# Performance work log

Hardware: AMD Instinct MI355X
Metric: run time of the kernel (lower is better)

## Reference

```python
import jax, jax.numpy as jnp
import numpy as np

B, N, C = 2, 2048, 1024
H = 16
D = C // H  # 64 head_dim
SCALE = D ** -0.5


def setup_inputs() -> dict:
    key = jax.random.key(0)
    k1, k2, k3 = jax.random.split(key, 3)
    x = jax.random.normal(k1, (B, N, C), dtype=jnp.float32)
    w_qkv = jax.random.normal(k2, (C, 3 * C), dtype=jnp.float32) * (C ** -0.5)
    w_proj = jax.random.normal(k3, (C, C), dtype=jnp.float32) * (C ** -0.5)
    b_proj = jnp.zeros((C,), dtype=jnp.float32)
    return {"x": x, "w_qkv": w_qkv, "w_proj": w_proj, "b_proj": b_proj}


def reference(x, w_qkv, w_proj, b_proj):
    # qkv projection (no bias, qkv_bias=False)
    qkv = x @ w_qkv                                   # [B,N,3C]
    qkv = qkv.reshape(B, N, 3, H, D)
    qkv = jnp.transpose(qkv, (2, 0, 3, 1, 4))         # [3,B,H,N,D]
    q, k, v = qkv[0], qkv[1], qkv[2]
    # scaled dot-product attention (full softmax == chunked loop in original)
    scores = jnp.einsum('bhqd,bhkd->bhqk', q, k) * SCALE
    attn = jax.nn.softmax(scores, axis=-1)
    out = jnp.einsum('bhqk,bhkd->bhqd', attn, v)      # [B,H,N,D]
    out = jnp.transpose(out, (0, 2, 1, 3)).reshape(B, N, C)
    return out @ w_proj + b_proj
```

## Files before the change

### kernel.cpp

```cpp
#include <hip/hip_runtime.h>
#include <stdint.h>

typedef float f32x4 __attribute__((ext_vector_type(4)));
typedef float f32x16 __attribute__((ext_vector_type(16)));
typedef __bf16 bf16x8 __attribute__((ext_vector_type(8)));
typedef unsigned int u32x4 __attribute__((ext_vector_type(4)));
typedef unsigned short u16x4 __attribute__((ext_vector_type(4)));

#define DEV __device__ __forceinline__

#define QSCALE_LOG2E 0.18033688011112042f

DEV unsigned short f2bf(float f) {
    unsigned u = __builtin_bit_cast(unsigned, f);
    u += 0x7fffu + ((u >> 16) & 1u);
    return (unsigned short)(u >> 16);
}

DEV unsigned pack2bf(float a, float b) {
    unsigned short ua = __builtin_bit_cast(unsigned short, (__bf16)a);
    unsigned short ub = __builtin_bit_cast(unsigned short, (__bf16)b);
    return (unsigned)ua | ((unsigned)ub << 16);
}

DEV void pswap(unsigned& a, unsigned& b) {
    asm volatile("v_permlane32_swap_b32 %0, %1" : "+v"(a), "+v"(b));
}

DEV void gload16(const void* g, void* l) {
    __builtin_amdgcn_global_load_lds(
        (const __attribute__((address_space(1))) unsigned int*)(uintptr_t)g,
        (__attribute__((address_space(3))) unsigned int*)(unsigned int)(uintptr_t)l,
        16, 0, 0);
}

__global__ void k_cvt(const float* __restrict__ in, unsigned short* __restrict__ out, int n4) {
    int i = blockIdx.x * 256 + threadIdx.x;
    int st = gridDim.x * 256;
    for (; i < n4; i += st) {
        f32x4 v = *(const f32x4*)(in + (size_t)i * 4);
        u16x4 o;
        o[0] = f2bf(v[0]); o[1] = f2bf(v[1]); o[2] = f2bf(v[2]); o[3] = f2bf(v[3]);
        *(u16x4*)(out + (size_t)i * 4) = o;
    }
}

__global__ void k_transpose(const float* __restrict__ in, unsigned short* __restrict__ out, int Nc) {
    __shared__ unsigned short tl[64][68];
    int n0 = blockIdx.x * 64, k0 = blockIdx.y * 64;
#pragma unroll
    for (int i = 0; i < 16; i++) {
        int idx = i * 256 + threadIdx.x;
        int kr = idx >> 6, nc = idx & 63;
        tl[kr][nc] = f2bf(in[(size_t)(k0 + kr) * Nc + n0 + nc]);
    }
    __syncthreads();
#pragma unroll
    for (int i = 0; i < 8; i++) {
        int idx = i * 256 + threadIdx.x;
        int nr = idx >> 5, kp2 = idx & 31;
        unsigned vv = (unsigned)tl[kp2 * 2][nr] | ((unsigned)tl[kp2 * 2 + 1][nr] << 16);
        *(unsigned*)(out + (size_t)(n0 + nr) * 1024 + k0 + kp2 * 2) = vv;
    }
}

template <int MODE>
__global__ __launch_bounds__(256) void k_gemm(
    const unsigned short* __restrict__ A, const unsigned short* __restrict__ Bt, int K,
    unsigned short* __restrict__ q, unsigned short* __restrict__ kk_,
    unsigned short* __restrict__ vT, const float* __restrict__ bias,
    float* __restrict__ outf) {
    __shared__ unsigned short As[2][128 * 64];
    __shared__ unsigned short Bs[2][128 * 64];
    const int tid = threadIdx.x;
    const int w = tid >> 6, l = tid & 63, g = l >> 4, lr = l & 15;
    const int wr = w >> 1, wc = w & 1;
    const int nwg = gridDim.x * gridDim.y, cpx = nwg >> 3;
    const int lin = blockIdx.y * gridDim.x + blockIdx.x;
    const int swz = (lin & 7) * cpx + (lin >> 3);
    const int m0 = (swz / gridDim.x) * 128, n0 = (swz % gridDim.x) * 128;
    f32x4 acc[4][4] = {};

    auto STAGE = [&](int buf, int k0) {
#pragma unroll
        for (int i = 0; i < 4; i++) {
            int c = i * 256 + tid;
            gload16(A + (size_t)(m0 + (c >> 3)) * K + k0 + (c & 7) * 8, (char*)As[buf] + c * 16);
            gload16(Bt + (size_t)(n0 + (c >> 3)) * K + k0 + (c & 7) * 8, (char*)Bs[buf] + c * 16);
        }
    };

    STAGE(0, 0);
    asm volatile("s_waitcnt vmcnt(0)" ::: "memory");
    __builtin_amdgcn_s_barrier();
    __builtin_amdgcn_sched_barrier(0);

    int cur = 0;
    for (int k0 = 0; k0 < K; k0 += 64) {
        if (k0 + 64 < K) STAGE(cur ^ 1, k0 + 64);
        const unsigned short* Ac = As[cur];
        const unsigned short* Bc = Bs[cur];
#pragma unroll
        for (int kk = 0; kk < 2; kk++) {
            bf16x8 af[4], bfv[4];
#pragma unroll
            for (int mi = 0; mi < 4; mi++)
                af[mi] = *(const bf16x8*)(Ac + (wr * 64 + mi * 16 + lr) * 64 + kk * 32 + g * 8);
#pragma unroll
            for (int ni = 0; ni < 4; ni++)
                bfv[ni] = *(const bf16x8*)(Bc + (wc * 64 + ni * 16 + lr) * 64 + kk * 32 + g * 8);
#pragma unroll
            for (int mi = 0; mi < 4; mi++)
#pragma unroll
                for (int ni = 0; ni < 4; ni++)
                    acc[mi][ni] = __builtin_amdgcn_mfma_f32_16x16x32_bf16(af[mi], bfv[ni], acc[mi][ni], 0, 0, 0);
        }
        asm volatile("s_waitcnt vmcnt(0)" ::: "memory");
        __builtin_amdgcn_s_barrier();
        __builtin_amdgcn_sched_barrier(0);
        cur ^= 1;
    }

#pragma unroll
    for (int mi = 0; mi < 4; mi++) {
#pragma unroll
        for (int ni = 0; ni < 4; ni++) {
            if (MODE == 1) {
                int row0 = m0 + wr * 64 + mi * 16 + g * 4;
                int col = n0 + wc * 64 + ni * 16 + lr;
                int b = row0 >> 11, nn = row0 & 2047;
                int which = col >> 10, cc = col & 1023;
                int h = cc >> 6, d = cc & 63;
                if (which == 2) {
                    u16x4 pv;
#pragma unroll
                    for (int r = 0; r < 4; r++) pv[r] = f2bf(acc[mi][ni][r]);
                    *(u16x4*)&vT[((size_t)(b * 16 + h) * 64 + d) * 2048 + nn] = pv;
                } else {
                    unsigned short* dst = (which == 0) ? q : kk_;
                    const float sc = (which == 0) ? QSCALE_LOG2E : 1.f;
#pragma unroll
                    for (int r = 0; r < 4; r++)
                        dst[((size_t)(b * 16 + h) * 2048 + nn + r) * 64 + d] = f2bf(acc[mi][ni][r] * sc);
                }
            } else {
#pragma unroll
                for (int r = 0; r < 4; r++) {
                    int row = m0 + wr * 64 + mi * 16 + g * 4 + r;
                    int col = n0 + wc * 64 + ni * 16 + lr;
                    outf[(size_t)row * 1024 + col] = acc[mi][ni][r] + bias[col];
                }
            }
        }
    }
}

__global__ __launch_bounds__(512, 2) void k_attn(
    const unsigned short* __restrict__ qb, const unsigned short* __restrict__ kb,
    const unsigned short* __restrict__ vTb, unsigned short* __restrict__ ao) {
    __shared__ __align__(16) char smem[49152];
    const int tid = threadIdx.x;
    const int w = tid >> 6, l = tid & 63, l31 = l & 31, hf = l >> 5;
    const int bid = blockIdx.x;
    const int xcd = bid & 7, slot = bid >> 3;
    const int bh = xcd * 4 + (slot >> 3), qb_ = slot & 7;
    const int b = bh >> 4, h = bh & 15;
    const unsigned short* qp = qb + (size_t)bh * 131072;
    const unsigned short* kp = kb + (size_t)bh * 131072;
    const unsigned short* vTp = vTb + (size_t)bh * 131072;

    const int qrow = qb_ * 256 + w * 32 + l31;
    bf16x8 qf[4];
#pragma unroll
    for (int dc = 0; dc < 4; dc++)
        qf[dc] = *(const bf16x8*)(qp + (size_t)qrow * 64 + dc * 16 + hf * 8);
    asm volatile("s_waitcnt vmcnt(0)" ::: "memory");

    f32x16 o_acc[2] = {};
    float l_r = 0.f;

    const int sr8 = l >> 3;
    const int sco = ((l & 7) ^ sr8) * 8;
    auto STAGE = [&](char* dst, int kv0) {
        gload16(kp + (size_t)(kv0 + w * 8 + sr8) * 64 + sco, dst + w * 1024 + (size_t)l * 16);
        gload16(vTp + (size_t)(w * 8 + sr8) * 2048 + kv0 + sco, dst + 8192 + w * 1024 + (size_t)l * 16);
    };

    char* p0 = smem;
    char* p1 = smem + 16384;
    char* p2 = smem + 32768;

    STAGE(p0, 0);
    STAGE(p1, 64);
    asm volatile("s_waitcnt vmcnt(2)" ::: "memory");
    __builtin_amdgcn_s_barrier();
    __builtin_amdgcn_sched_barrier(0);

    const int lb = l31 & 7;
    for (int t = 0; t < 32; ++t) {
        if (t < 30) STAGE(p2, (t + 2) * 64);

        f32x16 s[2] = {};
        __builtin_amdgcn_s_setprio(1);
#pragma unroll
        for (int kt = 0; kt < 2; kt++)
#pragma unroll
            for (int dc = 0; dc < 4; dc++) {
                bf16x8 kf = *(const bf16x8*)(p0 + (kt * 32 + l31) * 128 + (((2 * dc + hf) ^ lb) * 16));
                s[kt] = __builtin_amdgcn_mfma_f32_32x32x16_bf16(kf, qf[dc], s[kt], 0, 0, 0);
            }
        __builtin_amdgcn_s_setprio(0);

        float s0 = 0.f, s1 = 0.f, s2 = 0.f, s3 = 0.f;
#pragma unroll
        for (int kt = 0; kt < 2; kt++)
#pragma unroll
            for (int r = 0; r < 16; r += 4) {
                float e0 = __builtin_amdgcn_exp2f(s[kt][r]);
                float e1 = __builtin_amdgcn_exp2f(s[kt][r + 1]);
                float e2 = __builtin_amdgcn_exp2f(s[kt][r + 2]);
                float e3 = __builtin_amdgcn_exp2f(s[kt][r + 3]);
                s[kt][r] = e0; s[kt][r + 1] = e1; s[kt][r + 2] = e2; s[kt][r + 3] = e3;
                s0 += e0; s1 += e1; s2 += e2; s3 += e3;
            }
        float ssum = (s0 + s1) + (s2 + s3);
        ssum += __shfl_xor(ssum, 32);
        l_r += ssum;

        bf16x8 pf[4];
#pragma unroll
        for (int kt = 0; kt < 2; kt++) {
            unsigned wd[8];
#pragma unroll
            for (int i = 0; i < 8; i++) wd[i] = pack2bf(s[kt][2 * i], s[kt][2 * i + 1]);
#pragma unroll
            for (int cl = 0; cl < 2; cl++) {
                unsigned b0 = wd[4 * cl + 0], b2 = wd[4 * cl + 2];
                unsigned b1 = wd[4 * cl + 1], b3 = wd[4 * cl + 3];
                pswap(b0, b2);
                pswap(b1, b3);
                u32x4 bw; bw[0] = b0; bw[1] = b1; bw[2] = b2; bw[3] = b3;
                pf[2 * kt + cl] = __builtin_bit_cast(bf16x8, bw);
            }
        }

        __builtin_amdgcn_s_setprio(1);
#pragma unroll
        for (int c4 = 0; c4 < 4; c4++)
#pragma unroll
            for (int dt = 0; dt < 2; dt++) {
                bf16x8 vf = *(const bf16x8*)(p0 + 8192 + (dt * 32 + l31) * 128 + (((2 * c4 + hf) ^ lb) * 16));
                o_acc[dt] = __builtin_amdgcn_mfma_f32_32x32x16_bf16(vf, pf[c4], o_acc[dt], 0, 0, 0);
            }
        __builtin_amdgcn_s_setprio(0);

        if (t < 30)      asm volatile("s_waitcnt vmcnt(2)" ::: "memory");
        else if (t == 30) asm volatile("s_waitcnt vmcnt(0)" ::: "memory");
        if (t < 31) {
            __builtin_amdgcn_s_barrier();
            __builtin_amdgcn_sched_barrier(0);
        }
        char* tp = p0; p0 = p1; p1 = p2; p2 = tp;
    }

    float linv = 1.f / l_r;
    unsigned short* aop = ao + ((size_t)b * 2048 + qrow) * 1024 + h * 64;
#pragma unroll
    for (int dt = 0; dt < 2; dt++)
#pragma unroll
        for (int rg = 0; rg < 4; rg++) {
            u16x4 pv;
#pragma unroll
            for (int k = 0; k < 4; k++) pv[k] = f2bf(o_acc[dt][4 * rg + k] * linv);
            *(u16x4*)(aop + 8 * rg + 4 * hf + 32 * dt) = pv;
        }
}

extern "C" void kernel_launch(void* const* d_in, const int* in_sizes, int n_in,
                              void* d_out, int out_size, void* d_ws, size_t ws_size,
                              hipStream_t stream) {
    (void)in_sizes; (void)n_in; (void)out_size; (void)ws_size;
    const float* x      = (const float*)d_in[0];
    const float* w_qkv  = (const float*)d_in[1];
    const float* w_proj = (const float*)d_in[2];
    const float* b_proj = (const float*)d_in[3];
    float* out = (float*)d_out;
    char* ws = (char*)d_ws;

    unsigned short* xb     = (unsigned short*)(ws);
    unsigned short* ao     = (unsigned short*)(ws);
    unsigned short* wqkvT  = (unsigned short*)(ws + 8388608);
    unsigned short* wprojT = (unsigned short*)(ws + 14680064);
    unsigned short* qb     = (unsigned short*)(ws + 16777216);
    unsigned short* kb     = (unsigned short*)(ws + 25165824);
    unsigned short* vTb    = (unsigned short*)(ws + 33554432);

    k_cvt<<<2048, 256, 0, stream>>>(x, xb, 1048576);
    k_transpose<<<dim3(48, 16), 256, 0, stream>>>(w_qkv, wqkvT, 3072);
    k_transpose<<<dim3(16, 16), 256, 0, stream>>>(w_proj, wprojT, 1024);
    k_gemm<1><<<dim3(24, 32), 256, 0, stream>>>(xb, wqkvT, 1024, qb, kb, vTb, nullptr, nullptr);
    k_attn<<<256, 512, 0, stream>>>(qb, kb, vTb, ao);
    k_gemm<3><<<dim3(8, 32), 256, 0, stream>>>(ao, wprojT, 1024, nullptr, nullptr, nullptr, b_proj, out);
}
```

Measured before the change: 123.1 us.

## Split attention KV range across two wave groups and merge partials in LDS

The attention kernel now gives each block 128 query rows instead of 256, so twice as many blocks are launched. Inside a block, the 8 waves form two groups that each handle half of the key/value sequence, with double buffering in place of triple buffering. Partial outputs and row sums are combined through shared memory at the end, which is valid because no running max is used. The goal is more parallelism across the 256 CUs and better occupancy, at the cost of a final LDS reduction, two more block-wide barriers, and 64KB of shared memory per block.

```diff
diff --git a/kernel.cpp b/kernel.cpp
--- a/kernel.cpp
+++ b/kernel.cpp
@@ -155,21 +155,22 @@
     }
 }
 
-__global__ __launch_bounds__(512, 2) void k_attn(
+__global__ __launch_bounds__(512, 4) void k_attn(
     const unsigned short* __restrict__ qb, const unsigned short* __restrict__ kb,
     const unsigned short* __restrict__ vTb, unsigned short* __restrict__ ao) {
-    __shared__ __align__(16) char smem[49152];
+    __shared__ __align__(16) char smem[65536];
     const int tid = threadIdx.x;
     const int w = tid >> 6, l = tid & 63, l31 = l & 31, hf = l >> 5;
+    const int qg = w & 3, kvh = w >> 2;
     const int bid = blockIdx.x;
     const int xcd = bid & 7, slot = bid >> 3;
-    const int bh = xcd * 4 + (slot >> 3), qb_ = slot & 7;
+    const int bh = xcd * 4 + (slot >> 4), qb_ = slot & 15;
     const int b = bh >> 4, h = bh & 15;
     const unsigned short* qp = qb + (size_t)bh * 131072;
-    const unsigned short* kp = kb + (size_t)bh * 131072;
-    const unsigned short* vTp = vTb + (size_t)bh * 131072;
-
-    const int qrow = qb_ * 256 + w * 32 + l31;
+    const unsigned short* kp = kb + (size_t)bh * 131072 + (size_t)kvh * 65536;
+    const unsigned short* vTp = vTb + (size_t)bh * 131072 + kvh * 1024;
+
+    const int qrow = qb_ * 128 + qg * 32 + l31;
     bf16x8 qf[4];
 #pragma unroll
     for (int dc = 0; dc < 4; dc++)
@@ -181,24 +182,26 @@
 
     const int sr8 = l >> 3;
     const int sco = ((l & 7) ^ sr8) * 8;
+    char* sbase = smem + kvh * 32768;
     auto STAGE = [&](char* dst, int kv0) {
-        gload16(kp + (size_t)(kv0 + w * 8 + sr8) * 64 + sco, dst + w * 1024 + (size_t)l * 16);
-        gload16(vTp + (size_t)(w * 8 + sr8) * 2048 + kv0 + sco, dst + 8192 + w * 1024 + (size_t)l * 16);
+#pragma unroll
+        for (int i = 0; i < 2; i++) {
+            int r = qg + 4 * i;
+            gload16(kp + (size_t)(kv0 + r * 8 + sr8) * 64 + sco, dst + r * 1024 + (size_t)l * 16);
+            gload16(vTp + (size_t)(r * 8 + sr8) * 2048 + kv0 + sco, dst + 8192 + r * 1024 + (size_t)l * 16);
+        }
     };
 
-    char* p0 = smem;
-    char* p1 = smem + 16384;
-    char* p2 = smem + 32768;
-
-    STAGE(p0, 0);
-    STAGE(p1, 64);
-    asm volatile("s_waitcnt vmcnt(2)" ::: "memory");
+    STAGE(sbase, 0);
+    asm volatile("s_waitcnt vmcnt(0)" ::: "memory");
     __builtin_amdgcn_s_barrier();
     __builtin_amdgcn_sched_barrier(0);
 
     const int lb = l31 & 7;
-    for (int t = 0; t < 32; ++t) {
-        if (t < 30) STAGE(p2, (t + 2) * 64);
+    int cur = 0;
+    for (int t = 0; t < 16; ++t) {
+        if (t < 15) STAGE(sbase + (cur ^ 1) * 16384, (t + 1) * 64);
+        const char* p0 = sbase + cur * 16384;
 
         f32x16 s[2] = {};
         __builtin_amdgcn_s_setprio(1);
@@ -254,26 +257,41 @@
             }
         __builtin_amdgcn_s_setprio(0);
 
-        if (t < 30)      asm volatile("s_waitcnt vmcnt(2)" ::: "memory");
-        else if (t == 30) asm volatile("s_waitcnt vmcnt(0)" ::: "memory");
-        if (t < 31) {
+        if (t < 15) {
+            asm volatile("s_waitcnt vmcnt(0)" ::: "memory");
             __builtin_amdgcn_s_barrier();
             __builtin_amdgcn_sched_barrier(0);
         }
-        char* tp = p0; p0 = p1; p1 = p2; p2 = tp;
-    }
-
-    float linv = 1.f / l_r;
-    unsigned short* aop = ao + ((size_t)b * 2048 + qrow) * 1024 + h * 64;
-#pragma unroll
-    for (int dt = 0; dt < 2; dt++)
-#pragma unroll
-        for (int rg = 0; rg < 4; rg++) {
-            u16x4 pv;
-#pragma unroll
-            for (int k = 0; k < 4; k++) pv[k] = f2bf(o_acc[dt][4 * rg + k] * linv);
-            *(u16x4*)(aop + 8 * rg + 4 * hf + 32 * dt) = pv;
-        }
+        cur ^= 1;
+    }
+
+    __syncthreads();
+    float* dO = (float*)(smem + qg * 8704);
+    float* dL = (float*)(smem + 34816 + qg * 256);
+    if (kvh == 1) {
+#pragma unroll
+        for (int i = 0; i < 16; i++) dO[l * 34 + i] = o_acc[0][i];
+#pragma unroll
+        for (int i = 0; i < 16; i++) dO[l * 34 + 16 + i] = o_acc[1][i];
+        dL[l] = l_r;
+    }
+    __syncthreads();
+    if (kvh == 0) {
+        float linv = 1.f / (l_r + dL[l]);
+        unsigned short* aop = ao + ((size_t)b * 2048 + qrow) * 1024 + h * 64;
+#pragma unroll
+        for (int dt = 0; dt < 2; dt++)
+#pragma unroll
+            for (int rg = 0; rg < 4; rg++) {
+                u16x4 pv;
+#pragma unroll
+                for (int k = 0; k < 4; k++) {
+                    int r = rg * 4 + k;
+                    pv[k] = f2bf((o_acc[dt][r] + dO[l * 34 + dt * 16 + r]) * linv);
+                }
+                *(u16x4*)(aop + 8 * rg + 4 * hf + 32 * dt) = pv;
+            }
+    }
 }
 
 extern "C" void kernel_launch(void* const* d_in, const int* in_sizes, int n_in,
@@ -299,6 +317,6 @@
     k_transpose<<<dim3(48, 16), 256, 0, stream>>>(w_qkv, wqkvT, 3072);
     k_transpose<<<dim3(16, 16), 256, 0, stream>>>(w_proj, wprojT, 1024);
     k_gemm<1><<<dim3(24, 32), 256, 0, stream>>>(xb, wqkvT, 1024, qb, kb, vTb, nullptr, nullptr);
-    k_attn<<<256, 512, 0, stream>>>(qb, kb, vTb, ao);
+    k_attn<<<512, 512, 0, stream>>>(qb, kb, vTb, ao);
     k_gemm<3><<<dim3(8, 32), 256, 0, stream>>>(ao, wprojT, 1024, nullptr, nullptr, nullptr, b_proj, out);
 }
```

Measured after the change: 124.2 us. Within noise of the previous version (+1.0%).
